# Performance work log

Hardware: AMD Instinct MI355X
Metric: run time of the kernel (lower is better)

## Reference

```python
import jax, jax.numpy as jnp
import numpy as np

N_NODES = 50000
N_EDGES = 1600000
IN_DIM = 128
HEADS = 8
OUT_C = 16  # per-head channels; HEADS*OUT_C == IN_DIM -> residual active
NEG_SLOPE = 0.2
BN_EPS = 1e-5


def setup_inputs() -> dict:
    key = jax.random.key(0)
    ks = jax.random.split(key, 8)
    x = jax.random.normal(ks[0], (N_NODES, IN_DIM), dtype=jnp.float32)
    edge_index = jax.random.randint(ks[1], (2, N_EDGES), 0, N_NODES, dtype=jnp.int64)
    # GATConv params (PyG: shared lin for src/dst on single-tensor input)
    W = jax.random.normal(ks[2], (IN_DIM, HEADS * OUT_C), dtype=jnp.float32) / np.sqrt(IN_DIM)
    att_src = jax.random.normal(ks[3], (HEADS, OUT_C), dtype=jnp.float32) / np.sqrt(OUT_C)
    att_dst = jax.random.normal(ks[4], (HEADS, OUT_C), dtype=jnp.float32) / np.sqrt(OUT_C)
    bias = jnp.zeros((HEADS * OUT_C,), dtype=jnp.float32)
    # BatchNorm1d affine params
    gamma = jnp.ones((HEADS * OUT_C,), dtype=jnp.float32)
    beta = jnp.zeros((HEADS * OUT_C,), dtype=jnp.float32)
    return {"x": x, "edge_index": edge_index, "W": W, "att_src": att_src,
            "att_dst": att_dst, "bias": bias, "gamma": gamma, "beta": beta}


def reference(x, edge_index, W, att_src, att_dst, bias, gamma, beta):
    N = x.shape[0]
    H, C = att_src.shape
    src, dst = edge_index[0], edge_index[1]

    xl = (x @ W).reshape(N, H, C)                      # [N,H,C]
    a_src = jnp.sum(xl * att_src[None], axis=-1)       # [N,H]
    a_dst = jnp.sum(xl * att_dst[None], axis=-1)       # [N,H]

    e = jax.nn.leaky_relu(a_src[src] + a_dst[dst], NEG_SLOPE)  # [E,H]
    # segment softmax over incoming edges of each dst node
    m = jax.ops.segment_max(e, dst, num_segments=N)    # [N,H], -inf for empty
    m = jnp.where(jnp.isfinite(m), m, 0.0)
    ex = jnp.exp(e - m[dst])                           # [E,H]
    denom = jax.ops.segment_sum(ex, dst, num_segments=N)
    alpha = ex / (denom[dst] + 1e-16)                  # [E,H]

    out = jax.ops.segment_sum(alpha[:, :, None] * xl[src], dst, num_segments=N)  # [N,H,C]
    h = out.reshape(N, H * C) + bias

    # BatchNorm1d (training mode: batch statistics, biased variance)
    mean = jnp.mean(h, axis=0)
    var = jnp.mean((h - mean) ** 2, axis=0)
    h = (h - mean) * jax.lax.rsqrt(var + BN_EPS) * gamma + beta

    h = jax.nn.relu(h)
    return x + h  # residual (in_dim == H*C)
```

## Files before the change

kernel.cpp:

```cpp
#include <hip/hip_runtime.h>
#include <hip/hip_fp16.h>
#include <math.h>

#define N_NODES 50000
#define N_EDGES 1600000
#define DIM 128
#define HEADS 8
#define NEG_SLOPE 0.2f
#define BN_EPS 1e-5f

typedef _Float16 f16x8 __attribute__((ext_vector_type(8)));
typedef float f32x4 __attribute__((ext_vector_type(4)));

#define NBUCK 391
#define BSEGCAP 4864
#define CHUNK 8192
#define NB_A ((N_EDGES + CHUNK - 1) / CHUNK)
#define LIN_NB ((N_NODES + 127) / 128)
#define P1_NB (NB_A + LIN_NB)

struct BinAShm {
    int hist[NBUCK], excl[NBUCK], cnt2[NBUCK];
    int sc[512];
    unsigned int buf[CHUNK];
};
struct LinShm { __half wh[16384]; };

__device__ __forceinline__ void lin_block(
        int linb, const float* __restrict__ x, const float* __restrict__ W,
        const float* __restrict__ att_s, const float* __restrict__ att_d,
        __half* __restrict__ xlh, float* __restrict__ a_src,
        float* __restrict__ a_dst, __half* wh) {
    const int t = threadIdx.x;
    for (int v = t; v < 2048; v += 512) {
        const int g = v >> 6, lane = v & 63;
        const int nt = g >> 2, kt = g & 3;
        const int q = lane >> 4, n = lane & 15;
        #pragma unroll
        for (int j = 0; j < 8; ++j)
            wh[(size_t)(g * 64 + lane) * 8 + j] =
                __float2half(W[(kt * 32 + q * 8 + j) * DIM + nt * 16 + n]);
    }
    __syncthreads();

    const int wave = t >> 6;
    const int lane = t & 63;
    const int q = lane >> 4, n = lane & 15;
    const int nb = (linb * 8 + wave) * 16;

    const int rowA = min(nb + n, N_NODES - 1);
    const float* xr = x + (size_t)rowA * DIM;
    f16x8 a[4];
    #pragma unroll
    for (int kt = 0; kt < 4; ++kt) {
        const float4 p0 = *(const float4*)(xr + kt * 32 + q * 8);
        const float4 p1 = *(const float4*)(xr + kt * 32 + q * 8 + 4);
        a[kt][0] = (_Float16)p0.x; a[kt][1] = (_Float16)p0.y;
        a[kt][2] = (_Float16)p0.z; a[kt][3] = (_Float16)p0.w;
        a[kt][4] = (_Float16)p1.x; a[kt][5] = (_Float16)p1.y;
        a[kt][6] = (_Float16)p1.z; a[kt][7] = (_Float16)p1.w;
    }

    f32x4 acc[8];
    #pragma unroll
    for (int nt = 0; nt < 8; ++nt) acc[nt] = (f32x4){0.f, 0.f, 0.f, 0.f};

    const f16x8* wb = (const f16x8*)wh;
    #pragma unroll
    for (int nt = 0; nt < 8; ++nt) {
        #pragma unroll
        for (int kt = 0; kt < 4; ++kt) {
            const f16x8 b = wb[(nt * 4 + kt) * 64 + lane];
            acc[nt] = __builtin_amdgcn_mfma_f32_16x16x32_f16(a[kt], b, acc[nt], 0, 0, 0);
        }
    }

    const int r0 = nb + q * 4;
    #pragma unroll
    for (int nt = 0; nt < 8; ++nt) {
        const float as = att_s[nt * 16 + n];
        const float ad = att_d[nt * 16 + n];
        #pragma unroll
        for (int r = 0; r < 4; ++r) {
            const int row = r0 + r;
            const float v = acc[nt][r];
            float s = v * as;
            float d = v * ad;
            #pragma unroll
            for (int off = 8; off; off >>= 1) {
                s += __shfl_xor(s, off, 16);
                d += __shfl_xor(d, off, 16);
            }
            if (row < N_NODES) {
                xlh[(size_t)row * DIM + nt * 16 + n] = __float2half(v);
                if (n == 0) {
                    a_src[row * HEADS + nt] = s * 1.44269504f;
                    a_dst[row * HEADS + nt] = d * 1.44269504f;
                }
            }
        }
    }
}

__global__ __launch_bounds__(512) void k_phase1(
        const float* __restrict__ x, const float* __restrict__ W,
        const float* __restrict__ att_s, const float* __restrict__ att_d,
        const int* __restrict__ ei, unsigned int* __restrict__ meta,
        unsigned int* __restrict__ pairs, __half* __restrict__ xlh,
        float* __restrict__ a_src, float* __restrict__ a_dst) {
    __shared__ union { BinAShm a; LinShm l; } sh;
    const int t = threadIdx.x;

    if (blockIdx.x < NB_A) {
        const int blk = blockIdx.x;
        const int base = blk * CHUNK;
        const int cnt = min(CHUNK, N_EDGES - base);

        for (int j = t; j < NBUCK; j += 512) { sh.a.hist[j] = 0; sh.a.cnt2[j] = 0; }
        __syncthreads();
        for (int i = t * 4; i < cnt; i += 2048) {
            const int4 dv = *(const int4*)(ei + N_EDGES + base + i);
            atomicAdd(&sh.a.hist[dv.x >> 7], 1);
            atomicAdd(&sh.a.hist[dv.y >> 7], 1);
            atomicAdd(&sh.a.hist[dv.z >> 7], 1);
            atomicAdd(&sh.a.hist[dv.w >> 7], 1);
        }
        __syncthreads();
        sh.a.sc[t] = (t < NBUCK) ? sh.a.hist[t] : 0;
        __syncthreads();
        for (int d = 1; d < 512; d <<= 1) {
            int xo = 0;
            if (t >= d) xo = sh.a.sc[t - d];
            __syncthreads();
            sh.a.sc[t] += xo;
            __syncthreads();
        }
        if (t < NBUCK) {
            const int ex = sh.a.sc[t] - sh.a.hist[t];
            sh.a.excl[t] = ex;
            meta[(size_t)blk * NBUCK + t] =
                (unsigned int)sh.a.hist[t] | ((unsigned int)ex << 16);
        }
        __syncthreads();
        for (int i = t * 4; i < cnt; i += 2048) {
            const int4 sv = *(const int4*)(ei + base + i);
            const int4 dv = *(const int4*)(ei + N_EDGES + base + i);
            const int ss[4] = {sv.x, sv.y, sv.z, sv.w};
            const int dd[4] = {dv.x, dv.y, dv.z, dv.w};
            #pragma unroll
            for (int k = 0; k < 4; ++k) {
                const int b = dd[k] >> 7;
                const int r = atomicAdd(&sh.a.cnt2[b], 1);
                sh.a.buf[sh.a.excl[b] + r] = (unsigned int)ss[k]
                    | ((unsigned int)(dd[k] & 127) << 16);
            }
        }
        __syncthreads();
        for (int i = t * 4; i < cnt; i += 2048)
            *(int4*)(pairs + base + i) = *(const int4*)(sh.a.buf + i);
    } else {
        lin_block(blockIdx.x - NB_A, x, W, att_s, att_d, xlh, a_src, a_dst, sh.l.wh);
    }
}

__global__ __launch_bounds__(1024) void k_binaggr(
        const unsigned int* __restrict__ pairs, const unsigned int* __restrict__ meta,
        const float* __restrict__ a_src, const float* __restrict__ a_dst,
        const __half* __restrict__ xlh, float* __restrict__ y,
        float* __restrict__ gsums) {
    __shared__ int la[NB_A], ea[NB_A];
    __shared__ int hist[128], excl[128], cnt2[128], sc[128];
    __shared__ unsigned short out[BSEGCAP];
    const int t = threadIdx.x;
    const int b = blockIdx.x;
    if (b == 0 && t < 256) gsums[t] = 0.f;

    if (t < NB_A) {
        const unsigned int m = meta[(size_t)t * NBUCK + b];
        la[t] = (int)(m & 0xFFFF);
        ea[t] = (int)(m >> 16);
    }
    if (t < 128) { hist[t] = 0; cnt2[t] = 0; }
    __syncthreads();

    const int wave = t >> 6, lane = t & 63;

    for (int r = wave; r < NB_A; r += 16) {
        const int len = la[r];
        const unsigned int* src = pairs + (size_t)r * CHUNK + ea[r];
        for (int j = lane; j < len; j += 64)
            atomicAdd(&hist[(src[j] >> 16) & 127], 1);
    }
    __syncthreads();
    if (t < 128) sc[t] = hist[t];
    __syncthreads();
    for (int d = 1; d < 128; d <<= 1) {
        int xo = 0;
        if (t < 128 && t >= d) xo = sc[t - d];
        __syncthreads();
        if (t < 128) sc[t] += xo;
        __syncthreads();
    }
    if (t < 128) excl[t] = sc[t] - hist[t];
    __syncthreads();

    for (int r = wave; r < NB_A; r += 16) {
        const int len = la[r];
        const unsigned int* src = pairs + (size_t)r * CHUNK + ea[r];
        for (int j = lane; j < len; j += 64) {
            const unsigned int u = src[j];
            const int dl = (u >> 16) & 127;
            const int p = atomicAdd(&cnt2[dl], 1);
            out[excl[dl] + p] = (unsigned short)(u & 0xFFFF);
        }
    }
    __syncthreads();

    const int g = lane >> 4;
    const int cl = lane & 15;
    const int h = cl >> 1;

    for (int k = 0; k < 8; ++k) {
        const int nl = k * 16 + wave;
        const int d = (b << 7) + nl;
        if (d >= N_NODES) continue;
        const int lo = excl[nl];
        const int hi = lo + hist[nl];
        const float ad = a_dst[d * HEADS + h];

        float acc[8];
        #pragma unroll
        for (int q = 0; q < 8; ++q) acc[q] = 0.f;
        float dsum = 0.f;

        int i = lo;
        for (; i + 16 <= hi; i += 16) {
            const int s0 = out[i + g];
            const int s1 = out[i + 4 + g];
            const int s2 = out[i + 8 + g];
            const int s3 = out[i + 12 + g];
            const float as0 = a_src[s0 * HEADS + h];
            const float as1 = a_src[s1 * HEADS + h];
            const float as2 = a_src[s2 * HEADS + h];
            const float as3 = a_src[s3 * HEADS + h];
            const f16x8 x0 = *(const f16x8*)(xlh + (size_t)s0 * DIM + cl * 8);
            const f16x8 x1 = *(const f16x8*)(xlh + (size_t)s1 * DIM + cl * 8);
            const f16x8 x2 = *(const f16x8*)(xlh + (size_t)s2 * DIM + cl * 8);
            const f16x8 x3 = *(const f16x8*)(xlh + (size_t)s3 * DIM + cl * 8);
            const float e0 = as0 + ad;
            const float e1 = as1 + ad;
            const float e2 = as2 + ad;
            const float e3 = as3 + ad;
            const float w0 = exp2f(fmaxf(e0, NEG_SLOPE * e0));
            const float w1 = exp2f(fmaxf(e1, NEG_SLOPE * e1));
            const float w2 = exp2f(fmaxf(e2, NEG_SLOPE * e2));
            const float w3 = exp2f(fmaxf(e3, NEG_SLOPE * e3));
            dsum += (w0 + w1) + (w2 + w3);
            #pragma unroll
            for (int q = 0; q < 8; ++q) acc[q] = fmaf(w0, (float)x0[q], acc[q]);
            #pragma unroll
            for (int q = 0; q < 8; ++q) acc[q] = fmaf(w1, (float)x1[q], acc[q]);
            #pragma unroll
            for (int q = 0; q < 8; ++q) acc[q] = fmaf(w2, (float)x2[q], acc[q]);
            #pragma unroll
            for (int q = 0; q < 8; ++q) acc[q] = fmaf(w3, (float)x3[q], acc[q]);
        }
        for (; i + 8 <= hi; i += 8) {
            const int s0 = out[i + g];
            const int s1 = out[i + 4 + g];
            const float as0 = a_src[s0 * HEADS + h];
            const float as1 = a_src[s1 * HEADS + h];
            const f16x8 x0 = *(const f16x8*)(xlh + (size_t)s0 * DIM + cl * 8);
            const f16x8 x1 = *(const f16x8*)(xlh + (size_t)s1 * DIM + cl * 8);
            const float e0 = as0 + ad;
            const float e1 = as1 + ad;
            const float w0 = exp2f(fmaxf(e0, NEG_SLOPE * e0));
            const float w1 = exp2f(fmaxf(e1, NEG_SLOPE * e1));
            dsum += w0 + w1;
            #pragma unroll
            for (int q = 0; q < 8; ++q) acc[q] = fmaf(w0, (float)x0[q], acc[q]);
            #pragma unroll
            for (int q = 0; q < 8; ++q) acc[q] = fmaf(w1, (float)x1[q], acc[q]);
        }
        for (; i < hi; i += 4) {
            const int idx = i + g;
            const int sv = out[min(idx, hi - 1)];
            const float e = a_src[sv * HEADS + h] + ad;
            const f16x8 xv = *(const f16x8*)(xlh + (size_t)sv * DIM + cl * 8);
            float w = exp2f(fmaxf(e, NEG_SLOPE * e));
            if (idx >= hi) w = 0.f;
            dsum += w;
            #pragma unroll
            for (int q = 0; q < 8; ++q) acc[q] = fmaf(w, (float)xv[q], acc[q]);
        }
        #pragma unroll
        for (int q = 0; q < 8; ++q) {
            acc[q] += __shfl_xor(acc[q], 16);
            acc[q] += __shfl_xor(acc[q], 32);
        }
        dsum += __shfl_xor(dsum, 16);
        dsum += __shfl_xor(dsum, 32);
        const float inv = 1.f / (dsum + 1e-16f);
        float2 o;
        o.x = acc[2 * g] * inv;
        o.y = acc[2 * g + 1] * inv;
        *(float2*)(y + (size_t)d * DIM + cl * 8 + g * 2) = o;
    }
}

__global__ void k_stats(const float* __restrict__ y, const float* __restrict__ bias,
                        float* __restrict__ gsums) {
    const int c = threadIdx.x;
    const float b = bias[c];
    float s = 0.f, ss = 0.f;
    for (int n = blockIdx.x; n < N_NODES; n += gridDim.x) {
        const float h = y[n * DIM + c] + b;
        s += h;
        ss += h * h;
    }
    atomicAdd(&gsums[c], s);
    atomicAdd(&gsums[DIM + c], ss);
}

__global__ void k_final(float* __restrict__ y, const float* __restrict__ x,
                        const float* __restrict__ sums, const float* __restrict__ sumsq,
                        const float* __restrict__ gamma, const float* __restrict__ beta,
                        const float* __restrict__ bias) {
    const int q = blockIdx.x * blockDim.x + threadIdx.x;
    const int cq = q & (DIM / 4 - 1);
    const float4 sm = ((const float4*)sums)[cq];
    const float4 sq = ((const float4*)sumsq)[cq];
    const float4 gm = ((const float4*)gamma)[cq];
    const float4 bt = ((const float4*)beta)[cq];
    const float4 bs = ((const float4*)bias)[cq];
    float4 v = ((const float4*)y)[q];
    const float4 xv = ((const float4*)x)[q];
    const float inv_n = 1.f / (float)N_NODES;
#define BNC(c) { const float mean = sm.c * inv_n;                         \
                 const float var = sq.c * inv_n - mean * mean;            \
                 const float sc = rsqrtf(var + BN_EPS) * gm.c;            \
                 const float sh = bt.c + (bs.c - mean) * sc;              \
                 v.c = xv.c + fmaxf(v.c * sc + sh, 0.f); }
    BNC(x) BNC(y) BNC(z) BNC(w)
#undef BNC
    ((float4*)y)[q] = v;
}

extern "C" void kernel_launch(void* const* d_in, const int* in_sizes, int n_in,
                              void* d_out, int out_size, void* d_ws, size_t ws_size,
                              hipStream_t stream) {
    const float* x     = (const float*)d_in[0];
    const int*   ei    = (const int*)  d_in[1];
    const float* W     = (const float*)d_in[2];
    const float* att_s = (const float*)d_in[3];
    const float* att_d = (const float*)d_in[4];
    const float* bias  = (const float*)d_in[5];
    const float* gamma = (const float*)d_in[6];
    const float* beta  = (const float*)d_in[7];
    float* y = (float*)d_out;

    __half* xlh  = (__half*)d_ws;
    float* a_src = (float*)(xlh + (size_t)N_NODES * DIM);
    float* a_dst = a_src + (size_t)N_NODES * HEADS;
    float* sums  = a_dst + (size_t)N_NODES * HEADS;
    float* sumsq = sums  + DIM;
    unsigned int* meta  = (unsigned int*)(sumsq + DIM);
    unsigned int* pairs = meta + (size_t)NB_A * NBUCK;

    k_phase1<<<P1_NB, 512, 0, stream>>>(x, W, att_s, att_d, ei, meta, pairs,
                                        xlh, a_src, a_dst);
    k_binaggr<<<NBUCK, 1024, 0, stream>>>(pairs, meta, a_src, a_dst, xlh, y, sums);
    k_stats<<<512, DIM, 0, stream>>>(y, bias, sums);
    k_final<<<(size_t)N_NODES * DIM / 4 / 256, 256, 0, stream>>>(y, x, sums, sumsq,
                                                                 gamma, beta, bias);
}
```

Baseline: 239.2 us.

## Split bucket sort and aggregation into separate kernels with global CSR

Splits the fused bin-and-aggregate kernel into a sorting kernel that writes a per-bucket CSR of source ids and node ranges to global memory, plus a separate aggregation kernel launching one wave per destination node. This targets the low occupancy and load imbalance of 391 large blocks each doing both the sort and the gather for 128 nodes. CHUNK is halved, doubling the phase-1 binning blocks. The cost is an extra launch and a global round trip for the CSR. Overflow beyond BSEGCAP is now clamped rather than written out of bounds.

```diff
diff --git a/kernel.cpp b/kernel.cpp
--- a/kernel.cpp
+++ b/kernel.cpp
@@ -14,7 +14,7 @@
 
 #define NBUCK 391
 #define BSEGCAP 4864
-#define CHUNK 8192
+#define CHUNK 4096
 #define NB_A ((N_EDGES + CHUNK - 1) / CHUNK)
 #define LIN_NB ((N_NODES + 127) / 128)
 #define P1_NB (NB_A + LIN_NB)
@@ -163,10 +163,9 @@
     }
 }
 
-__global__ __launch_bounds__(1024) void k_binaggr(
+__global__ __launch_bounds__(512) void k_binB(
         const unsigned int* __restrict__ pairs, const unsigned int* __restrict__ meta,
-        const float* __restrict__ a_src, const float* __restrict__ a_dst,
-        const __half* __restrict__ xlh, float* __restrict__ y,
+        unsigned short* __restrict__ csr, int2* __restrict__ nrange,
         float* __restrict__ gsums) {
     __shared__ int la[NB_A], ea[NB_A];
     __shared__ int hist[128], excl[128], cnt2[128], sc[128];
@@ -185,7 +184,7 @@
 
     const int wave = t >> 6, lane = t & 63;
 
-    for (int r = wave; r < NB_A; r += 16) {
+    for (int r = wave; r < NB_A; r += 8) {
         const int len = la[r];
         const unsigned int* src = pairs + (size_t)r * CHUNK + ea[r];
         for (int j = lane; j < len; j += 64)
@@ -201,111 +200,127 @@
         if (t < 128) sc[t] += xo;
         __syncthreads();
     }
-    if (t < 128) excl[t] = sc[t] - hist[t];
-    __syncthreads();
-
-    for (int r = wave; r < NB_A; r += 16) {
+    if (t < 128) {
+        excl[t] = sc[t] - hist[t];
+        const int node = (b << 7) + t;
+        if (node < N_NODES) {
+            int2 rg;
+            rg.x = b * BSEGCAP + excl[t];
+            rg.y = rg.x + hist[t];
+            nrange[node] = rg;
+        }
+    }
+    __syncthreads();
+    const int cnt = min(sc[127], BSEGCAP);
+
+    for (int r = wave; r < NB_A; r += 8) {
         const int len = la[r];
         const unsigned int* src = pairs + (size_t)r * CHUNK + ea[r];
         for (int j = lane; j < len; j += 64) {
             const unsigned int u = src[j];
             const int dl = (u >> 16) & 127;
             const int p = atomicAdd(&cnt2[dl], 1);
-            out[excl[dl] + p] = (unsigned short)(u & 0xFFFF);
-        }
-    }
-    __syncthreads();
-
+            const int pos = excl[dl] + p;
+            if (pos < BSEGCAP) out[pos] = (unsigned short)(u & 0xFFFF);
+        }
+    }
+    __syncthreads();
+    for (int i = t; i < cnt; i += 512)
+        csr[(size_t)b * BSEGCAP + i] = out[i];
+}
+
+#define AGG_NB (N_NODES / 4)
+
+__global__ void k_aggr9(const int2* __restrict__ nrange,
+                        const unsigned short* __restrict__ csr,
+                        const float* __restrict__ a_src, const float* __restrict__ a_dst,
+                        const __half* __restrict__ xlh, float* __restrict__ y) {
+    const int d = blockIdx.x * 4 + (threadIdx.x >> 6);
+    const int lane = threadIdx.x & 63;
     const int g = lane >> 4;
     const int cl = lane & 15;
     const int h = cl >> 1;
-
+    const int2 rg = nrange[d];
+    const int lo = rg.x, hi = rg.y;
+    const float ad = a_dst[d * HEADS + h];
+
+    float acc[8];
+    #pragma unroll
+    for (int k = 0; k < 8; ++k) acc[k] = 0.f;
+    float dsum = 0.f;
+
+    int i = lo;
+    for (; i + 16 <= hi; i += 16) {
+        const int s0 = csr[i + g];
+        const int s1 = csr[i + 4 + g];
+        const int s2 = csr[i + 8 + g];
+        const int s3 = csr[i + 12 + g];
+        const float as0 = a_src[s0 * HEADS + h];
+        const float as1 = a_src[s1 * HEADS + h];
+        const float as2 = a_src[s2 * HEADS + h];
+        const float as3 = a_src[s3 * HEADS + h];
+        const f16x8 x0 = *(const f16x8*)(xlh + (size_t)s0 * DIM + cl * 8);
+        const f16x8 x1 = *(const f16x8*)(xlh + (size_t)s1 * DIM + cl * 8);
+        const f16x8 x2 = *(const f16x8*)(xlh + (size_t)s2 * DIM + cl * 8);
+        const f16x8 x3 = *(const f16x8*)(xlh + (size_t)s3 * DIM + cl * 8);
+        const float e0 = as0 + ad;
+        const float e1 = as1 + ad;
+        const float e2 = as2 + ad;
+        const float e3 = as3 + ad;
+        const float w0 = exp2f(fmaxf(e0, NEG_SLOPE * e0));
+        const float w1 = exp2f(fmaxf(e1, NEG_SLOPE * e1));
+        const float w2 = exp2f(fmaxf(e2, NEG_SLOPE * e2));
+        const float w3 = exp2f(fmaxf(e3, NEG_SLOPE * e3));
+        dsum += (w0 + w1) + (w2 + w3);
+        #pragma unroll
+        for (int k = 0; k < 8; ++k) acc[k] = fmaf(w0, (float)x0[k], acc[k]);
+        #pragma unroll
+        for (int k = 0; k < 8; ++k) acc[k] = fmaf(w1, (float)x1[k], acc[k]);
+        #pragma unroll
+        for (int k = 0; k < 8; ++k) acc[k] = fmaf(w2, (float)x2[k], acc[k]);
+        #pragma unroll
+        for (int k = 0; k < 8; ++k) acc[k] = fmaf(w3, (float)x3[k], acc[k]);
+    }
+    for (; i + 8 <= hi; i += 8) {
+        const int s0 = csr[i + g];
+        const int s1 = csr[i + 4 + g];
+        const float as0 = a_src[s0 * HEADS + h];
+        const float as1 = a_src[s1 * HEADS + h];
+        const f16x8 x0 = *(const f16x8*)(xlh + (size_t)s0 * DIM + cl * 8);
+        const f16x8 x1 = *(const f16x8*)(xlh + (size_t)s1 * DIM + cl * 8);
+        const float e0 = as0 + ad;
+        const float e1 = as1 + ad;
+        const float w0 = exp2f(fmaxf(e0, NEG_SLOPE * e0));
+        const float w1 = exp2f(fmaxf(e1, NEG_SLOPE * e1));
+        dsum += w0 + w1;
+        #pragma unroll
+        for (int k = 0; k < 8; ++k) acc[k] = fmaf(w0, (float)x0[k], acc[k]);
+        #pragma unroll
+        for (int k = 0; k < 8; ++k) acc[k] = fmaf(w1, (float)x1[k], acc[k]);
+    }
+    for (; i < hi; i += 4) {
+        const int idx = i + g;
+        const int sv = csr[min(idx, hi - 1)];
+        const float e = a_src[sv * HEADS + h] + ad;
+        const f16x8 xv = *(const f16x8*)(xlh + (size_t)sv * DIM + cl * 8);
+        float w = exp2f(fmaxf(e, NEG_SLOPE * e));
+        if (idx >= hi) w = 0.f;
+        dsum += w;
+        #pragma unroll
+        for (int k = 0; k < 8; ++k) acc[k] = fmaf(w, (float)xv[k], acc[k]);
+    }
+    #pragma unroll
     for (int k = 0; k < 8; ++k) {
-        const int nl = k * 16 + wave;
-        const int d = (b << 7) + nl;
-        if (d >= N_NODES) continue;
-        const int lo = excl[nl];
-        const int hi = lo + hist[nl];
-        const float ad = a_dst[d * HEADS + h];
-
-        float acc[8];
-        #pragma unroll
-        for (int q = 0; q < 8; ++q) acc[q] = 0.f;
-        float dsum = 0.f;
-
-        int i = lo;
-        for (; i + 16 <= hi; i += 16) {
-            const int s0 = out[i + g];
-            const int s1 = out[i + 4 + g];
-            const int s2 = out[i + 8 + g];
-            const int s3 = out[i + 12 + g];
-            const float as0 = a_src[s0 * HEADS + h];
-            const float as1 = a_src[s1 * HEADS + h];
-            const float as2 = a_src[s2 * HEADS + h];
-            const float as3 = a_src[s3 * HEADS + h];
-            const f16x8 x0 = *(const f16x8*)(xlh + (size_t)s0 * DIM + cl * 8);
-            const f16x8 x1 = *(const f16x8*)(xlh + (size_t)s1 * DIM + cl * 8);
-            const f16x8 x2 = *(const f16x8*)(xlh + (size_t)s2 * DIM + cl * 8);
-            const f16x8 x3 = *(const f16x8*)(xlh + (size_t)s3 * DIM + cl * 8);
-            const float e0 = as0 + ad;
-            const float e1 = as1 + ad;
-            const float e2 = as2 + ad;
-            const float e3 = as3 + ad;
-            const float w0 = exp2f(fmaxf(e0, NEG_SLOPE * e0));
-            const float w1 = exp2f(fmaxf(e1, NEG_SLOPE * e1));
-            const float w2 = exp2f(fmaxf(e2, NEG_SLOPE * e2));
-            const float w3 = exp2f(fmaxf(e3, NEG_SLOPE * e3));
-            dsum += (w0 + w1) + (w2 + w3);
-            #pragma unroll
-            for (int q = 0; q < 8; ++q) acc[q] = fmaf(w0, (float)x0[q], acc[q]);
-            #pragma unroll
-            for (int q = 0; q < 8; ++q) acc[q] = fmaf(w1, (float)x1[q], acc[q]);
-            #pragma unroll
-            for (int q = 0; q < 8; ++q) acc[q] = fmaf(w2, (float)x2[q], acc[q]);
-            #pragma unroll
-            for (int q = 0; q < 8; ++q) acc[q] = fmaf(w3, (float)x3[q], acc[q]);
-        }
-        for (; i + 8 <= hi; i += 8) {
-            const int s0 = out[i + g];
-            const int s1 = out[i + 4 + g];
-            const float as0 = a_src[s0 * HEADS + h];
-            const float as1 = a_src[s1 * HEADS + h];
-            const f16x8 x0 = *(const f16x8*)(xlh + (size_t)s0 * DIM + cl * 8);
-            const f16x8 x1 = *(const f16x8*)(xlh + (size_t)s1 * DIM + cl * 8);
-            const float e0 = as0 + ad;
-            const float e1 = as1 + ad;
-            const float w0 = exp2f(fmaxf(e0, NEG_SLOPE * e0));
-            const float w1 = exp2f(fmaxf(e1, NEG_SLOPE * e1));
-            dsum += w0 + w1;
-            #pragma unroll
-            for (int q = 0; q < 8; ++q) acc[q] = fmaf(w0, (float)x0[q], acc[q]);
-            #pragma unroll
-            for (int q = 0; q < 8; ++q) acc[q] = fmaf(w1, (float)x1[q], acc[q]);
-        }
-        for (; i < hi; i += 4) {
-            const int idx = i + g;
-            const int sv = out[min(idx, hi - 1)];
-            const float e = a_src[sv * HEADS + h] + ad;
-            const f16x8 xv = *(const f16x8*)(xlh + (size_t)sv * DIM + cl * 8);
-            float w = exp2f(fmaxf(e, NEG_SLOPE * e));
-            if (idx >= hi) w = 0.f;
-            dsum += w;
-            #pragma unroll
-            for (int q = 0; q < 8; ++q) acc[q] = fmaf(w, (float)xv[q], acc[q]);
-        }
-        #pragma unroll
-        for (int q = 0; q < 8; ++q) {
-            acc[q] += __shfl_xor(acc[q], 16);
-            acc[q] += __shfl_xor(acc[q], 32);
-        }
-        dsum += __shfl_xor(dsum, 16);
-        dsum += __shfl_xor(dsum, 32);
-        const float inv = 1.f / (dsum + 1e-16f);
-        float2 o;
-        o.x = acc[2 * g] * inv;
-        o.y = acc[2 * g + 1] * inv;
-        *(float2*)(y + (size_t)d * DIM + cl * 8 + g * 2) = o;
-    }
+        acc[k] += __shfl_xor(acc[k], 16);
+        acc[k] += __shfl_xor(acc[k], 32);
+    }
+    dsum += __shfl_xor(dsum, 16);
+    dsum += __shfl_xor(dsum, 32);
+    const float inv = 1.f / (dsum + 1e-16f);
+    float2 o;
+    o.x = acc[2 * g] * inv;
+    o.y = acc[2 * g + 1] * inv;
+    *(float2*)(y + (size_t)d * DIM + cl * 8 + g * 2) = o;
 }
 
 __global__ void k_stats(const float* __restrict__ y, const float* __restrict__ bias,
@@ -364,12 +379,15 @@
     float* a_dst = a_src + (size_t)N_NODES * HEADS;
     float* sums  = a_dst + (size_t)N_NODES * HEADS;
     float* sumsq = sums  + DIM;
-    unsigned int* meta  = (unsigned int*)(sumsq + DIM);
+    int2*  nrange = (int2*)(sumsq + DIM);
+    unsigned int* meta  = (unsigned int*)(nrange + N_NODES);
     unsigned int* pairs = meta + (size_t)NB_A * NBUCK;
+    unsigned short* csr = (unsigned short*)(pairs + (size_t)NB_A * CHUNK);
 
     k_phase1<<<P1_NB, 512, 0, stream>>>(x, W, att_s, att_d, ei, meta, pairs,
                                         xlh, a_src, a_dst);
-    k_binaggr<<<NBUCK, 1024, 0, stream>>>(pairs, meta, a_src, a_dst, xlh, y, sums);
+    k_binB<<<NBUCK, 512, 0, stream>>>(pairs, meta, csr, nrange, sums);
+    k_aggr9<<<AGG_NB, 256, 0, stream>>>(nrange, csr, a_src, a_dst, xlh, y);
     k_stats<<<512, DIM, 0, stream>>>(y, bias, sums);
     k_final<<<(size_t)N_NODES * DIM / 4 / 256, 256, 0, stream>>>(y, x, sums, sumsq,
                                                                  gamma, beta, bias);
```

Result: slower. 263.1 us (+10.0%).
